# Optimization experiments

Measured on AMD Instinct MI355X. Metric: run time of the kernel, lower is better.

Reference implementation:

```python
import jax, jax.numpy as jnp
import numpy as np

B, H, W, C = 32, 512, 512, 3


def dct2_matrix(N):
    # Orthonormal DCT-II basis: D[k, n] = s_k * sqrt(2/N) * cos(pi*(2n+1)*k/(2N))
    n = np.arange(N)
    k = n[:, None]
    D = np.cos(np.pi * (2 * n[None, :] + 1) * k / (2.0 * N)) * np.sqrt(2.0 / N)
    D[0, :] *= 1.0 / np.sqrt(2.0)  # ortho scaling of DC row
    return jnp.asarray(D, dtype=jnp.float32)


def setup_inputs() -> dict:
    key = jax.random.key(0)
    x = jax.random.normal(key, (B, H, W, C), dtype=jnp.float32)
    return {"x": x}


def reference(x) -> jnp.ndarray:
    # 2D DCT-II (ortho) along height and width, channels untouched.
    Dh = dct2_matrix(x.shape[1])  # [H, H]
    Dw = dct2_matrix(x.shape[2])  # [W, W]
    y = jnp.einsum('kh,bhwc->bkwc', Dh, x)   # DCT over height
    y = jnp.einsum('lw,bkwc->bklc', Dw, y)   # DCT over width
    return y
```

## Files before the change

kernel.cpp:

```cpp
#include <hip/hip_runtime.h>
#include <stdint.h>


typedef __bf16 bf16_t;
typedef bf16_t bf16x8 __attribute__((ext_vector_type(8)));
typedef float  f32x4  __attribute__((ext_vector_type(4)));

__device__ __forceinline__ uint32_t f2bf(float f) {
    union { float f; uint32_t u; } v; v.f = f;
    uint32_t r = v.u + 0x7fffu + ((v.u >> 16) & 1u);
    return r >> 16;
}

__device__ __forceinline__ f32x4 mfma16(bf16x8 a, bf16x8 b, f32x4 c) {
    return __builtin_amdgcn_mfma_f32_16x16x32_bf16(a, b, c, 0, 0, 0);
}

__device__ __forceinline__ void load_lds16(const void* g, void* l) {
    __builtin_amdgcn_global_load_lds(
        (const __attribute__((address_space(1))) uint32_t*)g,
        (__attribute__((address_space(3))) uint32_t*)l, 16, 0, 0);
}

__global__ __launch_bounds__(256) void gen_dct(uint16_t* __restrict__ Dbf) {
    int idx = blockIdx.x * 256 + threadIdx.x;
    int k = idx >> 9, h = idx & 511;
    int phase = ((2 * h + 1) * k) & 2047;
    float ang = (float)phase * 3.0679615757712823e-3f;
    float s = (k == 0) ? 0.04419417382415922f : 0.0625f;
    Dbf[idx] = (uint16_t)f2bf(__cosf(ang) * s);
}

__global__ __launch_bounds__(256, 4) void pass1(const float* __restrict__ x,
                                                const uint16_t* __restrict__ Dbf,
                                                uint16_t* __restrict__ Y) {
    __shared__ __align__(16) uint16_t Alds[2][128 * 32];
    __shared__ __align__(16) uint16_t Blds[2][96 * 32];
    const int t = threadIdx.x;
    const int lane = t & 63, wv = t >> 6;
    const int nt = blockIdx.x;
    const int mt = blockIdx.y;
    const int b  = blockIdx.z;
    const float* xb = x + (size_t)b * (512 * 1536);

    const int q0 = t, q1 = t + 256;
    const int m0 = q0 >> 2, i0 = (q0 & 3) ^ ((m0 >> 1) & 3);
    const int m1 = q1 >> 2, i1 = (q1 & 3) ^ ((m1 >> 1) & 3);
    const uint16_t* Asrc0 = Dbf + (size_t)(mt * 128 + m0) * 512 + i0 * 8;
    const uint16_t* Asrc1 = Dbf + (size_t)(mt * 128 + m1) * 512 + i1 * 8;

    const int jl = t % 96;
    const int hh = t / 96;
    const int wl = jl / 3, cc = jl - 3 * wl;
    const int ncol = cc * 32 + ((wl >> 1) + ((wl & 1) << 4));
    const int xv = (ncol >> 1) & 3;
    const int jg = nt * 96 + jl;
    const float* xsrc = xb + (size_t)(hh * 16) * 1536 + jg;

    f32x4 acc[2][6] = {};
    float v[16];

    load_lds16(Asrc0, &Alds[0][q0 * 8]);
    load_lds16(Asrc1, &Alds[0][q1 * 8]);
    if (t < 192) {
#pragma unroll
        for (int r = 0; r < 16; ++r) v[r] = xsrc[(size_t)r * 1536];
        uint32_t p[8];
#pragma unroll
        for (int i = 0; i < 8; ++i)
            p[i] = f2bf(v[2 * i]) | (f2bf(v[2 * i + 1]) << 16);
        *(uint4*)&Blds[0][ncol * 32 + (((hh * 2 + 0) ^ xv) << 3)] =
            make_uint4(p[0], p[1], p[2], p[3]);
        *(uint4*)&Blds[0][ncol * 32 + (((hh * 2 + 1) ^ xv) << 3)] =
            make_uint4(p[4], p[5], p[6], p[7]);
    }
    __syncthreads();

    for (int kt = 0; kt < 16; ++kt) {
        const int cur = kt & 1, nxt = cur ^ 1;

        if (kt < 15) {
            load_lds16(Asrc0 + (kt + 1) * 32, &Alds[nxt][q0 * 8]);
            load_lds16(Asrc1 + (kt + 1) * 32, &Alds[nxt][q1 * 8]);
            if (t < 192) {
                const float* s = xsrc + (size_t)(kt + 1) * 32 * 1536;
#pragma unroll
                for (int r = 0; r < 16; ++r) v[r] = s[(size_t)r * 1536];
            }
        }

        bf16x8 aq[2];
#pragma unroll
        for (int i = 0; i < 2; ++i) {
            int row = (wv * 2 + i) * 16 + (lane & 15);
            aq[i] = *(bf16x8*)&Alds[cur][row * 32 +
                        (((lane >> 4) ^ ((row >> 1) & 3)) << 3)];
        }
#pragma unroll
        for (int tt = 0; tt < 6; ++tt) {
            int col = tt * 16 + (lane & 15);
            bf16x8 bq = *(bf16x8*)&Blds[cur][col * 32 +
                        (((lane >> 4) ^ ((col >> 1) & 3)) << 3)];
            acc[0][tt] = mfma16(aq[0], bq, acc[0][tt]);
            acc[1][tt] = mfma16(aq[1], bq, acc[1][tt]);
        }

        if (kt < 15 && t < 192) {
            uint32_t p[8];
#pragma unroll
            for (int i = 0; i < 8; ++i)
                p[i] = f2bf(v[2 * i]) | (f2bf(v[2 * i + 1]) << 16);
            *(uint4*)&Blds[nxt][ncol * 32 + (((hh * 2 + 0) ^ xv) << 3)] =
                make_uint4(p[0], p[1], p[2], p[3]);
            *(uint4*)&Blds[nxt][ncol * 32 + (((hh * 2 + 1) ^ xv) << 3)] =
                make_uint4(p[4], p[5], p[6], p[7]);
        }
        __syncthreads();
    }

    const int wg = nt * 32 + 2 * (lane & 15);
#pragma unroll
    for (int i = 0; i < 2; ++i) {
        int kg = mt * 128 + (wv * 2 + i) * 16 + ((lane >> 4) << 2);
#pragma unroll
        for (int c = 0; c < 3; ++c)
#pragma unroll
            for (int r = 0; r < 4; ++r) {
                uint32_t pk = f2bf(acc[i][2 * c][r]) | (f2bf(acc[i][2 * c + 1][r]) << 16);
                *(uint32_t*)&Y[(size_t)b * 786432 + (size_t)(kg + r) * 1536 + c * 512 + wg] = pk;
            }
    }
}

__global__ __launch_bounds__(256, 4) void pass2(const uint16_t* __restrict__ Y,
                                                const uint16_t* __restrict__ Dbf,
                                                float* __restrict__ out) {
    __shared__ __align__(16) char smem[28672];
    const int t = threadIdx.x;
    const int lane = t & 63, wv = t >> 6;
    const int lt = blockIdx.x;
    const int mt = blockIdx.y;
    const int b  = blockIdx.z;
    const size_t yb = (size_t)b * 786432;

    const int qa0 = t;
    const int ma0 = qa0 >> 2, ia0 = (qa0 & 3) ^ ((ma0 >> 1) & 3);
    const int qa1 = t + 256;
    const int ma1 = qa1 >> 2, ia1 = (qa1 & 3) ^ ((ma1 >> 1) & 3);
    const int mb0 = ma0, ib0 = ia0;
    const int mb1 = ma1, ib1 = ia1;

    const uint16_t* As0 = Y + yb + (size_t)(mt * 96 + ma0) * 512 + ia0 * 8;
    const uint16_t* As1 = Y + yb + (size_t)(mt * 96 + ma1) * 512 + ia1 * 8;
    const uint16_t* Bs0 = Dbf + (size_t)(lt * 128 + mb0) * 512 + ib0 * 8;
    const uint16_t* Bs1 = Dbf + (size_t)(lt * 128 + mb1) * 512 + ib1 * 8;

    f32x4 acc[6][2] = {};

    auto stage = [&](int kt, int buf) {
        uint16_t* Al = (uint16_t*)(smem + buf * 14336);
        uint16_t* Bl = (uint16_t*)(smem + buf * 14336 + 6144);
        load_lds16(As0 + kt * 32, Al + qa0 * 8);
        if (t < 128) load_lds16(As1 + kt * 32, Al + qa1 * 8);
        load_lds16(Bs0 + kt * 32, Bl + qa0 * 8);
        load_lds16(Bs1 + kt * 32, Bl + qa1 * 8);
    };

    stage(0, 0);
    __syncthreads();

    for (int kt = 0; kt < 16; ++kt) {
        const int cur = kt & 1;
        if (kt < 15) stage(kt + 1, cur ^ 1);

        const uint16_t* Al = (const uint16_t*)(smem + cur * 14336);
        const uint16_t* Bl = (const uint16_t*)(smem + cur * 14336 + 6144);

        bf16x8 bq[2];
#pragma unroll
        for (int p = 0; p < 2; ++p) {
            int row = (wv * 2 + p) * 16 + (lane & 15);
            bq[p] = *(bf16x8*)&Bl[row * 32 +
                        (((lane >> 4) ^ ((row >> 1) & 3)) << 3)];
        }
#pragma unroll
        for (int tt = 0; tt < 6; ++tt) {
            int row = tt * 16 + (lane & 15);
            bf16x8 aq = *(bf16x8*)&Al[row * 32 +
                        (((lane >> 4) ^ ((row >> 1) & 3)) << 3)];
            acc[tt][0] = mfma16(aq, bq[0], acc[tt][0]);
            acc[tt][1] = mfma16(aq, bq[1], acc[tt][1]);
        }
        __syncthreads();
    }

    float* El = (float*)smem;
    const int kloc = t >> 3, sub = t & 7;
#pragma unroll
    for (int hf = 0; hf < 2; ++hf) {
        __syncthreads();
        if ((wv >> 1) == hf) {
#pragma unroll
            for (int tt = 0; tt < 6; ++tt)
#pragma unroll
                for (int p = 0; p < 2; ++p) {
                    int m = tt * 16 + ((lane >> 4) << 2);
                    int lc = ((wv & 1) * 2 + p) * 16 + (lane & 15);
#pragma unroll
                    for (int r = 0; r < 4; ++r)
                        El[(m + r) * 65 + lc] = acc[tt][p][r];
                }
        }
        __syncthreads();
        size_t ob = (size_t)b * 786432 + (size_t)(mt * 32 + kloc) * 1536 +
                    lt * 384 + hf * 192 + sub * 24;
#pragma unroll
        for (int q = 0; q < 6; ++q) {
            int o0 = hf * 192 + sub * 24 + q * 4;
            float4 v;
            v.x = El[(kloc * 3 + ((o0 + 0) % 3)) * 65 + ((o0 + 0) / 3 - hf * 64)];
            v.y = El[(kloc * 3 + ((o0 + 1) % 3)) * 65 + ((o0 + 1) / 3 - hf * 64)];
            v.z = El[(kloc * 3 + ((o0 + 2) % 3)) * 65 + ((o0 + 2) / 3 - hf * 64)];
            v.w = El[(kloc * 3 + ((o0 + 3) % 3)) * 65 + ((o0 + 3) / 3 - hf * 64)];
            *(float4*)&out[ob + q * 4] = v;
        }
    }
}

extern "C" void kernel_launch(void* const* d_in, const int* in_sizes, int n_in,
                              void* d_out, int out_size, void* d_ws, size_t ws_size,
                              hipStream_t stream) {
    (void)in_sizes; (void)n_in; (void)out_size; (void)ws_size;
    const float* x = (const float*)d_in[0];
    float* out = (float*)d_out;
    uint16_t* Dbf = (uint16_t*)d_ws;
    uint16_t* Y   = (uint16_t*)d_ws + 512 * 512;

    gen_dct<<<1024, 256, 0, stream>>>(Dbf);
    dim3 g1(16, 4, 32);
    pass1<<<g1, 256, 0, stream>>>(x, Dbf, Y);
    dim3 g2(4, 16, 32);
    pass2<<<g2, 256, 0, stream>>>(Y, Dbf, out);
}
```

Measured before the change: 277.6 us.

## Deepen software pipelining in both DCT passes with explicit waitcnt barriers

Pass 1 now double-buffers register prefetch of the fp32 input (two register sets) so global loads for step k+2 are in flight while step k is computed, and it replaces __syncthreads with explicit vmcnt/lgkmcnt waits plus raw s_barrier and sched_barrier fences. It also changes the LDS XOR swizzle for the B tile to a three-term hash to reduce bank conflicts. Pass 2 moves from a double to a triple-buffered LDS ring with prefetch depth two, raising shared memory use and lowering the launch-bounds occupancy hint from 4 to 3 blocks. The hand-counted vmcnt values are fragile, and the larger register and LDS footprint may cut occupancy.

```diff
diff --git a/kernel.cpp b/kernel.cpp
--- a/kernel.cpp
+++ b/kernel.cpp
@@ -5,6 +5,11 @@
 typedef __bf16 bf16_t;
 typedef bf16_t bf16x8 __attribute__((ext_vector_type(8)));
 typedef float  f32x4  __attribute__((ext_vector_type(4)));
+
+#define SCHED0 __builtin_amdgcn_sched_barrier(0)
+#define SBAR   __builtin_amdgcn_s_barrier()
+#define LGKM0  asm volatile("s_waitcnt lgkmcnt(0)" ::: "memory")
+#define VMW(n) asm volatile("s_waitcnt vmcnt(" #n ")" ::: "memory")
 
 __device__ __forceinline__ uint32_t f2bf(float f) {
     union { float f; uint32_t u; } v; v.f = f;
@@ -53,69 +58,84 @@
     const int hh = t / 96;
     const int wl = jl / 3, cc = jl - 3 * wl;
     const int ncol = cc * 32 + ((wl >> 1) + ((wl & 1) << 4));
-    const int xv = (ncol >> 1) & 3;
+    const int xv = ((ncol >> 1) ^ (ncol >> 3) ^ (ncol >> 5)) & 3;
     const int jg = nt * 96 + jl;
     const float* xsrc = xb + (size_t)(hh * 16) * 1536 + jg;
 
     f32x4 acc[2][6] = {};
-    float v[16];
-
-    load_lds16(Asrc0, &Alds[0][q0 * 8]);
-    load_lds16(Asrc1, &Alds[0][q1 * 8]);
-    if (t < 192) {
-#pragma unroll
-        for (int r = 0; r < 16; ++r) v[r] = xsrc[(size_t)r * 1536];
-        uint32_t p[8];
-#pragma unroll
-        for (int i = 0; i < 8; ++i)
-            p[i] = f2bf(v[2 * i]) | (f2bf(v[2 * i + 1]) << 16);
-        *(uint4*)&Blds[0][ncol * 32 + (((hh * 2 + 0) ^ xv) << 3)] =
-            make_uint4(p[0], p[1], p[2], p[3]);
-        *(uint4*)&Blds[0][ncol * 32 + (((hh * 2 + 1) ^ xv) << 3)] =
-            make_uint4(p[4], p[5], p[6], p[7]);
-    }
-    __syncthreads();
-
-    for (int kt = 0; kt < 16; ++kt) {
-        const int cur = kt & 1, nxt = cur ^ 1;
-
-        if (kt < 15) {
-            load_lds16(Asrc0 + (kt + 1) * 32, &Alds[nxt][q0 * 8]);
-            load_lds16(Asrc1 + (kt + 1) * 32, &Alds[nxt][q1 * 8]);
-            if (t < 192) {
-                const float* s = xsrc + (size_t)(kt + 1) * 32 * 1536;
-#pragma unroll
-                for (int r = 0; r < 16; ++r) v[r] = s[(size_t)r * 1536];
-            }
-        }
-
+    float vx0[16], vx1[16];
+
+    auto issueA = [&](int kk) {
+        load_lds16(Asrc0 + kk * 32, &Alds[kk & 1][q0 * 8]);
+        load_lds16(Asrc1 + kk * 32, &Alds[kk & 1][q1 * 8]);
+    };
+    auto issueX = [&](float (&vv)[16], int kk) {
+        if (t < 192) {
+            const float* s = xsrc + (size_t)kk * 32 * 1536;
+#pragma unroll
+            for (int r = 0; r < 16; ++r) vv[r] = s[(size_t)r * 1536];
+        }
+    };
+    auto packB = [&](const float (&vv)[16], int kk) {
+        if (t < 192) {
+            uint32_t p[8];
+#pragma unroll
+            for (int i = 0; i < 8; ++i)
+                p[i] = f2bf(vv[2 * i]) | (f2bf(vv[2 * i + 1]) << 16);
+            uint16_t* B = Blds[kk & 1];
+            *(uint4*)&B[ncol * 32 + (((hh * 2 + 0) ^ xv) << 3)] =
+                make_uint4(p[0], p[1], p[2], p[3]);
+            *(uint4*)&B[ncol * 32 + (((hh * 2 + 1) ^ xv) << 3)] =
+                make_uint4(p[4], p[5], p[6], p[7]);
+        }
+    };
+    auto compute = [&](int kk) {
+        const uint16_t* A  = Alds[kk & 1];
+        const uint16_t* Bl = Blds[kk & 1];
         bf16x8 aq[2];
 #pragma unroll
         for (int i = 0; i < 2; ++i) {
             int row = (wv * 2 + i) * 16 + (lane & 15);
-            aq[i] = *(bf16x8*)&Alds[cur][row * 32 +
+            aq[i] = *(const bf16x8*)&A[row * 32 +
                         (((lane >> 4) ^ ((row >> 1) & 3)) << 3)];
         }
 #pragma unroll
         for (int tt = 0; tt < 6; ++tt) {
             int col = tt * 16 + (lane & 15);
-            bf16x8 bq = *(bf16x8*)&Blds[cur][col * 32 +
-                        (((lane >> 4) ^ ((col >> 1) & 3)) << 3)];
+            int xr = ((col >> 1) ^ (col >> 3) ^ (col >> 5)) & 3;
+            bf16x8 bq = *(const bf16x8*)&Bl[col * 32 + (((lane >> 4) ^ xr) << 3)];
             acc[0][tt] = mfma16(aq[0], bq, acc[0][tt]);
             acc[1][tt] = mfma16(aq[1], bq, acc[1][tt]);
         }
-
-        if (kt < 15 && t < 192) {
-            uint32_t p[8];
-#pragma unroll
-            for (int i = 0; i < 8; ++i)
-                p[i] = f2bf(v[2 * i]) | (f2bf(v[2 * i + 1]) << 16);
-            *(uint4*)&Blds[nxt][ncol * 32 + (((hh * 2 + 0) ^ xv) << 3)] =
-                make_uint4(p[0], p[1], p[2], p[3]);
-            *(uint4*)&Blds[nxt][ncol * 32 + (((hh * 2 + 1) ^ xv) << 3)] =
-                make_uint4(p[4], p[5], p[6], p[7]);
-        }
-        __syncthreads();
+    };
+    auto endstep = [&](int kt) {
+        LGKM0;
+        if (kt <= 13 && t < 192) { VMW(16); }
+        else                     { VMW(0);  }
+        SBAR; SCHED0;
+    };
+
+    issueX(vx0, 0); SCHED0;
+    issueA(0);      SCHED0;
+    issueX(vx1, 1); SCHED0;
+    packB(vx0, 0);
+    endstep(0);
+
+    for (int k2 = 0; k2 < 8; ++k2) {
+        const int ke = 2 * k2, ko = ke + 1;
+        issueA(ko);                      SCHED0;
+        if (ke + 2 < 16) issueX(vx0, ke + 2);
+        SCHED0;
+        packB(vx1, ko);
+        compute(ke);
+        endstep(ke);
+        if (ko + 1 < 16) issueA(ko + 1);
+        SCHED0;
+        if (ko + 2 < 16) issueX(vx1, ko + 2);
+        SCHED0;
+        if (ko + 1 < 16) packB(vx0, ko + 1);
+        compute(ko);
+        if (ko < 15) endstep(ko);
     }
 
     const int wg = nt * 32 + 2 * (lane & 15);
@@ -132,10 +152,10 @@
     }
 }
 
-__global__ __launch_bounds__(256, 4) void pass2(const uint16_t* __restrict__ Y,
+__global__ __launch_bounds__(256, 3) void pass2(const uint16_t* __restrict__ Y,
                                                 const uint16_t* __restrict__ Dbf,
                                                 float* __restrict__ out) {
-    __shared__ __align__(16) char smem[28672];
+    __shared__ __align__(16) char smem[43008];
     const int t = threadIdx.x;
     const int lane = t & 63, wv = t >> 6;
     const int lt = blockIdx.x;
@@ -147,13 +167,11 @@
     const int ma0 = qa0 >> 2, ia0 = (qa0 & 3) ^ ((ma0 >> 1) & 3);
     const int qa1 = t + 256;
     const int ma1 = qa1 >> 2, ia1 = (qa1 & 3) ^ ((ma1 >> 1) & 3);
-    const int mb0 = ma0, ib0 = ia0;
-    const int mb1 = ma1, ib1 = ia1;
 
     const uint16_t* As0 = Y + yb + (size_t)(mt * 96 + ma0) * 512 + ia0 * 8;
     const uint16_t* As1 = Y + yb + (size_t)(mt * 96 + ma1) * 512 + ia1 * 8;
-    const uint16_t* Bs0 = Dbf + (size_t)(lt * 128 + mb0) * 512 + ib0 * 8;
-    const uint16_t* Bs1 = Dbf + (size_t)(lt * 128 + mb1) * 512 + ib1 * 8;
+    const uint16_t* Bs0 = Dbf + (size_t)(lt * 128 + ma0) * 512 + ia0 * 8;
+    const uint16_t* Bs1 = Dbf + (size_t)(lt * 128 + ma1) * 512 + ia1 * 8;
 
     f32x4 acc[6][2] = {};
 
@@ -165,35 +183,43 @@
         load_lds16(Bs0 + kt * 32, Bl + qa0 * 8);
         load_lds16(Bs1 + kt * 32, Bl + qa1 * 8);
     };
-
-    stage(0, 0);
-    __syncthreads();
-
-    for (int kt = 0; kt < 16; ++kt) {
-        const int cur = kt & 1;
-        if (kt < 15) stage(kt + 1, cur ^ 1);
-
-        const uint16_t* Al = (const uint16_t*)(smem + cur * 14336);
-        const uint16_t* Bl = (const uint16_t*)(smem + cur * 14336 + 6144);
-
+    auto compute = [&](int buf) {
+        const uint16_t* Al = (const uint16_t*)(smem + buf * 14336);
+        const uint16_t* Bl = (const uint16_t*)(smem + buf * 14336 + 6144);
         bf16x8 bq[2];
 #pragma unroll
         for (int p = 0; p < 2; ++p) {
             int row = (wv * 2 + p) * 16 + (lane & 15);
-            bq[p] = *(bf16x8*)&Bl[row * 32 +
+            bq[p] = *(const bf16x8*)&Bl[row * 32 +
                         (((lane >> 4) ^ ((row >> 1) & 3)) << 3)];
         }
 #pragma unroll
         for (int tt = 0; tt < 6; ++tt) {
             int row = tt * 16 + (lane & 15);
-            bf16x8 aq = *(bf16x8*)&Al[row * 32 +
+            bf16x8 aq = *(const bf16x8*)&Al[row * 32 +
                         (((lane >> 4) ^ ((row >> 1) & 3)) << 3)];
             acc[tt][0] = mfma16(aq, bq[0], acc[tt][0]);
             acc[tt][1] = mfma16(aq, bq[1], acc[tt][1]);
         }
-        __syncthreads();
-    }
-
+    };
+
+    stage(0, 0); SCHED0;
+    stage(1, 1); SCHED0;
+    if (t < 128) { VMW(4); } else { VMW(3); }
+    SBAR; SCHED0;
+
+    for (int kt = 0; kt < 16; ++kt) {
+        if (kt + 2 < 16) stage(kt + 2, (kt + 2) % 3);
+        SCHED0;
+        compute(kt % 3);
+        if (kt < 15) {
+            if (kt <= 13) { if (t < 128) { VMW(4); } else { VMW(3); } }
+            else          { VMW(0); }
+            SBAR; SCHED0;
+        }
+    }
+
+    __syncthreads();
     float* El = (float*)smem;
     const int kloc = t >> 3, sub = t & 7;
 #pragma unroll
```

Measured after the change: 278.2 us. Within noise of the previous version (+0.2%).

## Double K-tile depth to 64 and hand-schedule loads, waits and barriers

Applied to the files above, without the earlier changes.

Both GEMM passes now stage 64-wide K tiles instead of 32, so each loop runs 8 iterations with half as many barriers. The LDS swizzle is widened to 8 slots to match. Explicit sched_barrier, waitcnt and s_barrier calls replace __syncthreads so global loads overlap MFMA work, and s_setprio raises priority around the MFMA block. LDS use doubles and launch bounds drop to 2 blocks per CU, which lowers occupancy and raises register pressure from the 32 prefetched floats per thread.

```diff
diff --git a/kernel.cpp b/kernel.cpp
--- a/kernel.cpp
+++ b/kernel.cpp
@@ -5,6 +5,11 @@
 typedef __bf16 bf16_t;
 typedef bf16_t bf16x8 __attribute__((ext_vector_type(8)));
 typedef float  f32x4  __attribute__((ext_vector_type(4)));
+
+#define SCHED0 __builtin_amdgcn_sched_barrier(0)
+#define SBAR   __builtin_amdgcn_s_barrier()
+#define LGKM0  asm volatile("s_waitcnt lgkmcnt(0)" ::: "memory")
+#define VMW0   asm volatile("s_waitcnt vmcnt(0)" ::: "memory")
 
 __device__ __forceinline__ uint32_t f2bf(float f) {
     union { float f; uint32_t u; } v; v.f = f;
@@ -31,11 +36,11 @@
     Dbf[idx] = (uint16_t)f2bf(__cosf(ang) * s);
 }
 
-__global__ __launch_bounds__(256, 4) void pass1(const float* __restrict__ x,
+__global__ __launch_bounds__(256, 2) void pass1(const float* __restrict__ x,
                                                 const uint16_t* __restrict__ Dbf,
                                                 uint16_t* __restrict__ Y) {
-    __shared__ __align__(16) uint16_t Alds[2][128 * 32];
-    __shared__ __align__(16) uint16_t Blds[2][96 * 32];
+    __shared__ __align__(16) uint16_t Alds[2][128 * 64];
+    __shared__ __align__(16) uint16_t Blds[2][96 * 64];
     const int t = threadIdx.x;
     const int lane = t & 63, wv = t >> 6;
     const int nt = blockIdx.x;
@@ -43,79 +48,97 @@
     const int b  = blockIdx.z;
     const float* xb = x + (size_t)b * (512 * 1536);
 
-    const int q0 = t, q1 = t + 256;
-    const int m0 = q0 >> 2, i0 = (q0 & 3) ^ ((m0 >> 1) & 3);
-    const int m1 = q1 >> 2, i1 = (q1 & 3) ^ ((m1 >> 1) & 3);
-    const uint16_t* Asrc0 = Dbf + (size_t)(mt * 128 + m0) * 512 + i0 * 8;
-    const uint16_t* Asrc1 = Dbf + (size_t)(mt * 128 + m1) * 512 + i1 * 8;
+    const int qA0 = t, qA1 = t + 256, qA2 = t + 512, qA3 = t + 768;
+    const int mA0 = qA0 >> 3, gA0 = (qA0 & 7) ^ ((mA0 >> 1) & 7);
+    const int mA1 = qA1 >> 3, gA1 = (qA1 & 7) ^ ((mA1 >> 1) & 7);
+    const int mA2 = qA2 >> 3, gA2 = (qA2 & 7) ^ ((mA2 >> 1) & 7);
+    const int mA3 = qA3 >> 3, gA3 = (qA3 & 7) ^ ((mA3 >> 1) & 7);
+    const uint16_t* As0 = Dbf + (size_t)(mt * 128 + mA0) * 512 + gA0 * 8;
+    const uint16_t* As1 = Dbf + (size_t)(mt * 128 + mA1) * 512 + gA1 * 8;
+    const uint16_t* As2 = Dbf + (size_t)(mt * 128 + mA2) * 512 + gA2 * 8;
+    const uint16_t* As3 = Dbf + (size_t)(mt * 128 + mA3) * 512 + gA3 * 8;
 
     const int jl = t % 96;
     const int hh = t / 96;
     const int wl = jl / 3, cc = jl - 3 * wl;
     const int ncol = cc * 32 + ((wl >> 1) + ((wl & 1) << 4));
-    const int xv = (ncol >> 1) & 3;
+    const int xv = ((ncol >> 1) ^ (ncol >> 3) ^ (ncol >> 5)) & 7;
     const int jg = nt * 96 + jl;
-    const float* xsrc = xb + (size_t)(hh * 16) * 1536 + jg;
+    const float* xsrc = xb + (size_t)(hh * 32) * 1536 + jg;
 
     f32x4 acc[2][6] = {};
-    float v[16];
-
-    load_lds16(Asrc0, &Alds[0][q0 * 8]);
-    load_lds16(Asrc1, &Alds[0][q1 * 8]);
-    if (t < 192) {
-#pragma unroll
-        for (int r = 0; r < 16; ++r) v[r] = xsrc[(size_t)r * 1536];
-        uint32_t p[8];
-#pragma unroll
-        for (int i = 0; i < 8; ++i)
-            p[i] = f2bf(v[2 * i]) | (f2bf(v[2 * i + 1]) << 16);
-        *(uint4*)&Blds[0][ncol * 32 + (((hh * 2 + 0) ^ xv) << 3)] =
-            make_uint4(p[0], p[1], p[2], p[3]);
-        *(uint4*)&Blds[0][ncol * 32 + (((hh * 2 + 1) ^ xv) << 3)] =
-            make_uint4(p[4], p[5], p[6], p[7]);
-    }
-    __syncthreads();
-
-    for (int kt = 0; kt < 16; ++kt) {
-        const int cur = kt & 1, nxt = cur ^ 1;
-
-        if (kt < 15) {
-            load_lds16(Asrc0 + (kt + 1) * 32, &Alds[nxt][q0 * 8]);
-            load_lds16(Asrc1 + (kt + 1) * 32, &Alds[nxt][q1 * 8]);
-            if (t < 192) {
-                const float* s = xsrc + (size_t)(kt + 1) * 32 * 1536;
-#pragma unroll
-                for (int r = 0; r < 16; ++r) v[r] = s[(size_t)r * 1536];
-            }
-        }
-
-        bf16x8 aq[2];
+    float vx[32];
+
+    auto issueA = [&](int kk) {
+        uint16_t* A = Alds[kk & 1];
+        load_lds16(As0 + kk * 64, A + qA0 * 8);
+        load_lds16(As1 + kk * 64, A + qA1 * 8);
+        load_lds16(As2 + kk * 64, A + qA2 * 8);
+        load_lds16(As3 + kk * 64, A + qA3 * 8);
+    };
+    auto issueX = [&](int kk) {
+        if (t < 192) {
+            const float* s = xsrc + (size_t)kk * 64 * 1536;
+#pragma unroll
+            for (int r = 0; r < 32; ++r) vx[r] = s[(size_t)r * 1536];
+        }
+    };
+    auto packB = [&](int kk) {
+        if (t < 192) {
+            uint32_t p[16];
+#pragma unroll
+            for (int i = 0; i < 16; ++i)
+                p[i] = f2bf(vx[2 * i]) | (f2bf(vx[2 * i + 1]) << 16);
+            uint16_t* B = Blds[kk & 1];
+#pragma unroll
+            for (int u = 0; u < 4; ++u) {
+                int slot = (hh * 4 + u) ^ xv;
+                *(uint4*)&B[ncol * 64 + slot * 8] =
+                    make_uint4(p[4 * u], p[4 * u + 1], p[4 * u + 2], p[4 * u + 3]);
+            }
+        }
+    };
+    auto compute = [&](int kk) {
+        const uint16_t* A  = Alds[kk & 1];
+        const uint16_t* Bl = Blds[kk & 1];
+        bf16x8 aq[2][2];
 #pragma unroll
         for (int i = 0; i < 2; ++i) {
             int row = (wv * 2 + i) * 16 + (lane & 15);
-            aq[i] = *(bf16x8*)&Alds[cur][row * 32 +
-                        (((lane >> 4) ^ ((row >> 1) & 3)) << 3)];
-        }
+#pragma unroll
+            for (int ks = 0; ks < 2; ++ks) {
+                int slot = (ks * 4 + (lane >> 4)) ^ ((row >> 1) & 7);
+                aq[i][ks] = *(const bf16x8*)&A[row * 64 + slot * 8];
+            }
+        }
+        __builtin_amdgcn_s_setprio(1);
 #pragma unroll
         for (int tt = 0; tt < 6; ++tt) {
             int col = tt * 16 + (lane & 15);
-            bf16x8 bq = *(bf16x8*)&Blds[cur][col * 32 +
-                        (((lane >> 4) ^ ((col >> 1) & 3)) << 3)];
-            acc[0][tt] = mfma16(aq[0], bq, acc[0][tt]);
-            acc[1][tt] = mfma16(aq[1], bq, acc[1][tt]);
-        }
-
-        if (kt < 15 && t < 192) {
-            uint32_t p[8];
-#pragma unroll
-            for (int i = 0; i < 8; ++i)
-                p[i] = f2bf(v[2 * i]) | (f2bf(v[2 * i + 1]) << 16);
-            *(uint4*)&Blds[nxt][ncol * 32 + (((hh * 2 + 0) ^ xv) << 3)] =
-                make_uint4(p[0], p[1], p[2], p[3]);
-            *(uint4*)&Blds[nxt][ncol * 32 + (((hh * 2 + 1) ^ xv) << 3)] =
-                make_uint4(p[4], p[5], p[6], p[7]);
-        }
-        __syncthreads();
+            int xr = ((col >> 1) ^ (col >> 3) ^ (col >> 5)) & 7;
+#pragma unroll
+            for (int ks = 0; ks < 2; ++ks) {
+                int slot = (ks * 4 + (lane >> 4)) ^ xr;
+                bf16x8 bq = *(const bf16x8*)&Bl[col * 64 + slot * 8];
+                acc[0][tt] = mfma16(aq[0][ks], bq, acc[0][tt]);
+                acc[1][tt] = mfma16(aq[1][ks], bq, acc[1][tt]);
+            }
+        }
+        __builtin_amdgcn_s_setprio(0);
+    };
+
+    issueA(0); SCHED0;
+    issueX(0); SCHED0;
+    packB(0);
+    LGKM0; VMW0; SBAR; SCHED0;
+
+    for (int kt = 0; kt < 8; ++kt) {
+        if (kt < 7) { issueA(kt + 1); SCHED0; issueX(kt + 1); SCHED0; }
+        compute(kt);
+        if (kt < 7) {
+            packB(kt + 1);
+            LGKM0; VMW0; SBAR; SCHED0;
+        }
     }
 
     const int wg = nt * 32 + 2 * (lane & 15);
@@ -132,10 +155,10 @@
     }
 }
 
-__global__ __launch_bounds__(256, 4) void pass2(const uint16_t* __restrict__ Y,
+__global__ __launch_bounds__(256, 2) void pass2(const uint16_t* __restrict__ Y,
                                                 const uint16_t* __restrict__ Dbf,
                                                 float* __restrict__ out) {
-    __shared__ __align__(16) char smem[28672];
+    __shared__ __align__(16) char smem[57344];
     const int t = threadIdx.x;
     const int lane = t & 63, wv = t >> 6;
     const int lt = blockIdx.x;
@@ -143,57 +166,74 @@
     const int b  = blockIdx.z;
     const size_t yb = (size_t)b * 786432;
 
-    const int qa0 = t;
-    const int ma0 = qa0 >> 2, ia0 = (qa0 & 3) ^ ((ma0 >> 1) & 3);
-    const int qa1 = t + 256;
-    const int ma1 = qa1 >> 2, ia1 = (qa1 & 3) ^ ((ma1 >> 1) & 3);
-    const int mb0 = ma0, ib0 = ia0;
-    const int mb1 = ma1, ib1 = ia1;
-
-    const uint16_t* As0 = Y + yb + (size_t)(mt * 96 + ma0) * 512 + ia0 * 8;
-    const uint16_t* As1 = Y + yb + (size_t)(mt * 96 + ma1) * 512 + ia1 * 8;
-    const uint16_t* Bs0 = Dbf + (size_t)(lt * 128 + mb0) * 512 + ib0 * 8;
-    const uint16_t* Bs1 = Dbf + (size_t)(lt * 128 + mb1) * 512 + ib1 * 8;
+    const int qA0 = t, qA1 = t + 256, qA2 = t + 512;
+    const int mA0 = qA0 >> 3, gA0 = (qA0 & 7) ^ ((mA0 >> 1) & 7);
+    const int mA1 = qA1 >> 3, gA1 = (qA1 & 7) ^ ((mA1 >> 1) & 7);
+    const int mA2 = qA2 >> 3, gA2 = (qA2 & 7) ^ ((mA2 >> 1) & 7);
+    const int qB3 = t + 768;
+    const int mB3 = qB3 >> 3, gB3 = (qB3 & 7) ^ ((mB3 >> 1) & 7);
+
+    const uint16_t* Ys0 = Y + yb + (size_t)(mt * 96 + mA0) * 512 + gA0 * 8;
+    const uint16_t* Ys1 = Y + yb + (size_t)(mt * 96 + mA1) * 512 + gA1 * 8;
+    const uint16_t* Ys2 = Y + yb + (size_t)(mt * 96 + mA2) * 512 + gA2 * 8;
+    const uint16_t* Ds0 = Dbf + (size_t)(lt * 128 + mA0) * 512 + gA0 * 8;
+    const uint16_t* Ds1 = Dbf + (size_t)(lt * 128 + mA1) * 512 + gA1 * 8;
+    const uint16_t* Ds2 = Dbf + (size_t)(lt * 128 + mA2) * 512 + gA2 * 8;
+    const uint16_t* Ds3 = Dbf + (size_t)(lt * 128 + mB3) * 512 + gB3 * 8;
 
     f32x4 acc[6][2] = {};
 
-    auto stage = [&](int kt, int buf) {
-        uint16_t* Al = (uint16_t*)(smem + buf * 14336);
-        uint16_t* Bl = (uint16_t*)(smem + buf * 14336 + 6144);
-        load_lds16(As0 + kt * 32, Al + qa0 * 8);
-        if (t < 128) load_lds16(As1 + kt * 32, Al + qa1 * 8);
-        load_lds16(Bs0 + kt * 32, Bl + qa0 * 8);
-        load_lds16(Bs1 + kt * 32, Bl + qa1 * 8);
-    };
-
-    stage(0, 0);
-    __syncthreads();
-
-    for (int kt = 0; kt < 16; ++kt) {
-        const int cur = kt & 1;
-        if (kt < 15) stage(kt + 1, cur ^ 1);
-
-        const uint16_t* Al = (const uint16_t*)(smem + cur * 14336);
-        const uint16_t* Bl = (const uint16_t*)(smem + cur * 14336 + 6144);
-
-        bf16x8 bq[2];
+    auto stage = [&](int kt) {
+        const int buf = kt & 1;
+        uint16_t* Al = (uint16_t*)(smem + buf * 28672);
+        uint16_t* Bl = (uint16_t*)(smem + buf * 28672 + 12288);
+        load_lds16(Ys0 + kt * 64, Al + qA0 * 8);
+        load_lds16(Ys1 + kt * 64, Al + qA1 * 8);
+        load_lds16(Ys2 + kt * 64, Al + qA2 * 8);
+        load_lds16(Ds0 + kt * 64, Bl + qA0 * 8);
+        load_lds16(Ds1 + kt * 64, Bl + qA1 * 8);
+        load_lds16(Ds2 + kt * 64, Bl + qA2 * 8);
+        load_lds16(Ds3 + kt * 64, Bl + qB3 * 8);
+    };
+    auto compute = [&](int kt) {
+        const int buf = kt & 1;
+        const uint16_t* Al = (const uint16_t*)(smem + buf * 28672);
+        const uint16_t* Bl = (const uint16_t*)(smem + buf * 28672 + 12288);
+        bf16x8 bq[2][2];
 #pragma unroll
         for (int p = 0; p < 2; ++p) {
             int row = (wv * 2 + p) * 16 + (lane & 15);
-            bq[p] = *(bf16x8*)&Bl[row * 32 +
-                        (((lane >> 4) ^ ((row >> 1) & 3)) << 3)];
-        }
+#pragma unroll
+            for (int ks = 0; ks < 2; ++ks) {
+                int slot = (ks * 4 + (lane >> 4)) ^ ((row >> 1) & 7);
+                bq[p][ks] = *(const bf16x8*)&Bl[row * 64 + slot * 8];
+            }
+        }
+        __builtin_amdgcn_s_setprio(1);
 #pragma unroll
         for (int tt = 0; tt < 6; ++tt) {
             int row = tt * 16 + (lane & 15);
-            bf16x8 aq = *(bf16x8*)&Al[row * 32 +
-                        (((lane >> 4) ^ ((row >> 1) & 3)) << 3)];
-            acc[tt][0] = mfma16(aq, bq[0], acc[tt][0]);
-            acc[tt][1] = mfma16(aq, bq[1], acc[tt][1]);
-        }
-        __syncthreads();
-    }
-
+#pragma unroll
+            for (int ks = 0; ks < 2; ++ks) {
+                int slot = (ks * 4 + (lane >> 4)) ^ ((row >> 1) & 7);
+                bf16x8 aq = *(const bf16x8*)&Al[row * 64 + slot * 8];
+                acc[tt][0] = mfma16(aq, bq[0][ks], acc[tt][0]);
+                acc[tt][1] = mfma16(aq, bq[1][ks], acc[tt][1]);
+            }
+        }
+        __builtin_amdgcn_s_setprio(0);
+    };
+
+    stage(0); SCHED0;
+    VMW0; SBAR; SCHED0;
+
+    for (int kt = 0; kt < 8; ++kt) {
+        if (kt < 7) { stage(kt + 1); SCHED0; }
+        compute(kt);
+        if (kt < 7) { VMW0; SBAR; SCHED0; }
+    }
+
+    __syncthreads();
     float* El = (float*)smem;
     const int kloc = t >> 3, sub = t & 7;
 #pragma unroll
```

Result: slower. 291.1 us (+4.9%).
